# Optimization experiments

Hardware: AMD Instinct MI355X
Metric: run time of the kernel (lower is better)

Reference implementation:

```python
import jax, jax.numpy as jnp
import numpy as np

B = 256          # batch of images
TOK = 256        # 16x16 tokens per image
V = 1024         # codebook size
D = 256          # code dim


def setup_inputs() -> dict:
    key = jax.random.key(0)
    k1, k2, k3, k4 = jax.random.split(key, 4)
    image_seq = jax.random.randint(k1, (B, TOK), 0, V, dtype=jnp.int64)
    image_seq2 = jax.random.randint(k2, (B, TOK), 0, V, dtype=jnp.int64)
    alpha = jax.random.uniform(k3, (1,), dtype=jnp.float32)
    W = jax.random.normal(k4, (V, D), dtype=jnp.float32)
    return {"image_seq": image_seq, "image_seq2": image_seq2, "alpha": alpha, "W": W}


def reference(image_seq, image_seq2, alpha, W):
    a = alpha[0]
    # gather codebook entries: [B, TOK, D]
    emb = W[image_seq]
    emb2 = W[image_seq2]
    x = (1.0 - a) * emb + a * emb2
    xf = x.reshape(-1, D)                        # [N, D], N = B*TOK
    # brute-force L2 distance to every code, without materializing [N, V, D]:
    d = (jnp.sum(xf * xf, axis=-1, keepdims=True)
         - 2.0 * xf @ W.T
         + jnp.sum(W * W, axis=-1)[None, :])
    idx = jnp.argmin(d, axis=1)                  # top-1 nearest code, [N]
    # get_codebook_entry: gather, reshape to bhwc, permute to bchw
    z_q = W[idx].reshape(B, 16, 16, D)           # [B, 16, 16, 256]
    z_q = jnp.transpose(z_q, (0, 3, 1, 2))       # [B, 256, 16, 16]
    return z_q
```

## Files before the change

kernel.cpp:

```cpp
#include <hip/hip_runtime.h>

static constexpr int Vn = 1024;
static constexpr int Dn = 256;
static constexpr int NT = 65536;

typedef float vfloat4 __attribute__((ext_vector_type(4)));

__global__ __launch_bounds__(256) void gram_kernel(const float* __restrict__ W,
                                                   float* __restrict__ G,
                                                   float* __restrict__ norms) {
    __shared__ float As[32][33];
    __shared__ float Bs[32][33];
    const int tid = threadIdx.x;
    const int tx = tid & 15;
    const int ty = tid >> 4;
    const int bm = blockIdx.y * 32;
    const int bn = blockIdx.x * 32;
    float acc[2][2] = {};
    for (int k0 = 0; k0 < Dn; k0 += 32) {
#pragma unroll
        for (int s = 0; s < 4; ++s) {
            const int e = tid + 256 * s;
            const int m = e >> 5;
            const int k = e & 31;
            As[k][m] = W[(bm + m) * Dn + k0 + k];
            Bs[k][m] = W[(bn + m) * Dn + k0 + k];
        }
        __syncthreads();
#pragma unroll
        for (int kk = 0; kk < 32; ++kk) {
            float a[2], b[2];
#pragma unroll
            for (int u = 0; u < 2; ++u) a[u] = As[kk][ty + 16 * u];
#pragma unroll
            for (int w = 0; w < 2; ++w) b[w] = Bs[kk][tx + 16 * w];
#pragma unroll
            for (int u = 0; u < 2; ++u)
#pragma unroll
                for (int w = 0; w < 2; ++w)
                    acc[u][w] = fmaf(a[u], b[w], acc[u][w]);
        }
        __syncthreads();
    }
#pragma unroll
    for (int u = 0; u < 2; ++u) {
        const int row = bm + ty + 16 * u;
#pragma unroll
        for (int w = 0; w < 2; ++w) {
            const int col = bn + tx + 16 * w;
            G[row * Vn + col] = acc[u][w];
            if (row == col) norms[row] = acc[u][w];
        }
    }
}

__global__ __launch_bounds__(256) void argmin_write_kernel(const int* __restrict__ seq,
                                                           const int* __restrict__ seq2,
                                                           const float* __restrict__ alpha,
                                                           const float* __restrict__ G,
                                                           const float* __restrict__ norms,
                                                           const float* __restrict__ W,
                                                           float* __restrict__ out) {
    __shared__ float T[32][129];
    __shared__ int bestVs[32];
    const int tid = threadIdx.x;
    const int wave = tid >> 6;
    const int lane = tid & 63;
    const int t0 = blockIdx.x * 32;

    float4 nn_r[4];
#pragma unroll
    for (int s = 0; s < 4; ++s) nn_r[s] = ((const float4*)norms)[s * 64 + lane];

    const float a = alpha[0];
    const float c0 = -2.0f * (1.0f - a);
    const float c1 = -2.0f * a;

    for (int bb = 0; bb < 2; ++bb) {
        const int base_t = t0 + wave * 8 + bb * 4;
        const int base_l = wave * 8 + bb * 4;
        int iv[4], jv[4];
#pragma unroll
        for (int q = 0; q < 4; ++q) { iv[q] = seq[base_t + q]; jv[q] = seq2[base_t + q]; }
#pragma unroll
        for (int pair = 0; pair < 2; ++pair) {
            const int qa = pair * 2, qb = pair * 2 + 1;
            const float4* GiA = (const float4*)(G + iv[qa] * Vn);
            const float4* GjA = (const float4*)(G + jv[qa] * Vn);
            const float4* GiB = (const float4*)(G + iv[qb] * Vn);
            const float4* GjB = (const float4*)(G + jv[qb] * Vn);
            float4 gia[4], gja[4], gib[4], gjb[4];
#pragma unroll
            for (int s = 0; s < 4; ++s) {
                const int e = s * 64 + lane;
                gia[s] = GiA[e];
                gja[s] = GjA[e];
                gib[s] = GiB[e];
                gjb[s] = GjB[e];
            }
            float bestA = __builtin_inff(), bestB = __builtin_inff();
            int vA = 0, vB = 0;
#pragma unroll
            for (int s = 0; s < 4; ++s) {
                const int e = s * 64 + lane;
                const float4 nn = nn_r[s];
                const int v = e * 4;
                {
                    const float s0 = fmaf(c1, gja[s].x, fmaf(c0, gia[s].x, nn.x));
                    const float s1 = fmaf(c1, gja[s].y, fmaf(c0, gia[s].y, nn.y));
                    const float s2 = fmaf(c1, gja[s].z, fmaf(c0, gia[s].z, nn.z));
                    const float s3 = fmaf(c1, gja[s].w, fmaf(c0, gia[s].w, nn.w));
                    if (s0 < bestA) { bestA = s0; vA = v; }
                    if (s1 < bestA) { bestA = s1; vA = v + 1; }
                    if (s2 < bestA) { bestA = s2; vA = v + 2; }
                    if (s3 < bestA) { bestA = s3; vA = v + 3; }
                }
                {
                    const float s0 = fmaf(c1, gjb[s].x, fmaf(c0, gib[s].x, nn.x));
                    const float s1 = fmaf(c1, gjb[s].y, fmaf(c0, gib[s].y, nn.y));
                    const float s2 = fmaf(c1, gjb[s].z, fmaf(c0, gib[s].z, nn.z));
                    const float s3 = fmaf(c1, gjb[s].w, fmaf(c0, gib[s].w, nn.w));
                    if (s0 < bestB) { bestB = s0; vB = v; }
                    if (s1 < bestB) { bestB = s1; vB = v + 1; }
                    if (s2 < bestB) { bestB = s2; vB = v + 2; }
                    if (s3 < bestB) { bestB = s3; vB = v + 3; }
                }
            }
#pragma unroll
            for (int off = 32; off >= 1; off >>= 1) {
                const float oa = __shfl_down(bestA, off, 64);
                const int   va = __shfl_down(vA, off, 64);
                if (oa < bestA || (oa == bestA && va < vA)) { bestA = oa; vA = va; }
                const float ob = __shfl_down(bestB, off, 64);
                const int   vb = __shfl_down(vB, off, 64);
                if (ob < bestB || (ob == bestB && vb < vB)) { bestB = ob; vB = vb; }
            }
            if (lane == 0) {
                bestVs[base_l + qa] = vA;
                bestVs[base_l + qb] = vB;
            }
        }
    }
    __syncthreads();

    const int b   = t0 >> 8;
    const int hw0 = t0 & 255;
    float* outb = out + b * 65536 + hw0;
    const int tok = tid >> 3;
    const int l8  = tid & 7;
    const int hw4  = (tid & 7) * 4;
    const int drow = tid >> 3;
#pragma unroll
    for (int half = 0; half < 2; ++half) {
        const int v = bestVs[tok];
        const float4* Wr = (const float4*)(W + v * Dn + half * 128);
#pragma unroll
        for (int p = 0; p < 4; ++p) {
            const int d4 = p * 8 + l8;
            const float4 w4 = Wr[d4];
            T[tok][d4 * 4 + 0] = w4.x;
            T[tok][d4 * 4 + 1] = w4.y;
            T[tok][d4 * 4 + 2] = w4.z;
            T[tok][d4 * 4 + 3] = w4.w;
        }
        __syncthreads();
#pragma unroll
        for (int dp = 0; dp < 128; dp += 32) {
            const int dl = dp + drow;
            const int d = half * 128 + dl;
            vfloat4 o;
            o.x = T[hw4 + 0][dl];
            o.y = T[hw4 + 1][dl];
            o.z = T[hw4 + 2][dl];
            o.w = T[hw4 + 3][dl];
            __builtin_nontemporal_store(o, (vfloat4*)(outb + d * 256 + hw4));
        }
        __syncthreads();
    }
}

extern "C" void kernel_launch(void* const* d_in, const int* in_sizes, int n_in,
                              void* d_out, int out_size, void* d_ws, size_t ws_size,
                              hipStream_t stream) {
    const int*   seq   = (const int*)d_in[0];
    const int*   seq2  = (const int*)d_in[1];
    const float* alpha = (const float*)d_in[2];
    const float* W     = (const float*)d_in[3];
    float* out = (float*)d_out;

    char* ws = (char*)d_ws;
    float* G     = (float*)(ws);
    float* norms = (float*)(ws + 4194304);

    gram_kernel<<<dim3(32, 32), 256, 0, stream>>>(W, G, norms);
    argmin_write_kernel<<<NT / 32, 256, 0, stream>>>(seq, seq2, alpha, G, norms, W, out);
}
```

Before: 130.6 us.

## Enlarge Gram kernel tiles to 64x64 with register prefetch and vector loads

```diff
diff --git a/kernel.cpp b/kernel.cpp
--- a/kernel.cpp
+++ b/kernel.cpp
@@ -9,48 +9,70 @@
 __global__ __launch_bounds__(256) void gram_kernel(const float* __restrict__ W,
                                                    float* __restrict__ G,
                                                    float* __restrict__ norms) {
-    __shared__ float As[32][33];
-    __shared__ float Bs[32][33];
+    __shared__ float As[64][33];
+    __shared__ float Bs[64][33];
     const int tid = threadIdx.x;
     const int tx = tid & 15;
     const int ty = tid >> 4;
-    const int bm = blockIdx.y * 32;
-    const int bn = blockIdx.x * 32;
-    float acc[2][2] = {};
-    for (int k0 = 0; k0 < Dn; k0 += 32) {
-#pragma unroll
-        for (int s = 0; s < 4; ++s) {
-            const int e = tid + 256 * s;
-            const int m = e >> 5;
-            const int k = e & 31;
-            As[k][m] = W[(bm + m) * Dn + k0 + k];
-            Bs[k][m] = W[(bn + m) * Dn + k0 + k];
-        }
-        __syncthreads();
+    const int bm = blockIdx.y * 64;
+    const int bn = blockIdx.x * 64;
+    const float4* Wv = (const float4*)W;
+
+    const int m0  = tid >> 3;
+    const int kql = tid & 7;
+
+    float4 pa[2], pb[2];
+#pragma unroll
+    for (int s = 0; s < 2; ++s) {
+        pa[s] = Wv[(bm + m0 + 32 * s) * 64 + kql];
+        pb[s] = Wv[(bn + m0 + 32 * s) * 64 + kql];
+    }
+
+    float acc[4][4] = {};
+    for (int c = 0; c < 8; ++c) {
+#pragma unroll
+        for (int s = 0; s < 2; ++s) {
+            const int m = m0 + 32 * s;
+            As[m][kql * 4 + 0] = pa[s].x;
+            As[m][kql * 4 + 1] = pa[s].y;
+            As[m][kql * 4 + 2] = pa[s].z;
+            As[m][kql * 4 + 3] = pa[s].w;
+            Bs[m][kql * 4 + 0] = pb[s].x;
+            Bs[m][kql * 4 + 1] = pb[s].y;
+            Bs[m][kql * 4 + 2] = pb[s].z;
+            Bs[m][kql * 4 + 3] = pb[s].w;
+        }
+        __syncthreads();
+        if (c < 7) {
+            const int kq = (c + 1) * 8 + kql;
+#pragma unroll
+            for (int s = 0; s < 2; ++s) {
+                pa[s] = Wv[(bm + m0 + 32 * s) * 64 + kq];
+                pb[s] = Wv[(bn + m0 + 32 * s) * 64 + kq];
+            }
+        }
 #pragma unroll
         for (int kk = 0; kk < 32; ++kk) {
-            float a[2], b[2];
-#pragma unroll
-            for (int u = 0; u < 2; ++u) a[u] = As[kk][ty + 16 * u];
-#pragma unroll
-            for (int w = 0; w < 2; ++w) b[w] = Bs[kk][tx + 16 * w];
-#pragma unroll
-            for (int u = 0; u < 2; ++u)
-#pragma unroll
-                for (int w = 0; w < 2; ++w)
+            float a[4], b[4];
+#pragma unroll
+            for (int u = 0; u < 4; ++u) a[u] = As[ty * 4 + u][kk];
+#pragma unroll
+            for (int w = 0; w < 4; ++w) b[w] = Bs[tx * 4 + w][kk];
+#pragma unroll
+            for (int u = 0; u < 4; ++u)
+#pragma unroll
+                for (int w = 0; w < 4; ++w)
                     acc[u][w] = fmaf(a[u], b[w], acc[u][w]);
         }
         __syncthreads();
     }
 #pragma unroll
-    for (int u = 0; u < 2; ++u) {
-        const int row = bm + ty + 16 * u;
-#pragma unroll
-        for (int w = 0; w < 2; ++w) {
-            const int col = bn + tx + 16 * w;
-            G[row * Vn + col] = acc[u][w];
-            if (row == col) norms[row] = acc[u][w];
-        }
+    for (int u = 0; u < 4; ++u) {
+        const int row = bm + ty * 4 + u;
+        vfloat4 o;
+        o.x = acc[u][0]; o.y = acc[u][1]; o.z = acc[u][2]; o.w = acc[u][3];
+        *(vfloat4*)(G + row * Vn + bn + tx * 4) = o;
+        if (bm == bn && tx == ty) norms[row] = acc[u][u];
     }
 }
 
@@ -192,6 +214,6 @@
     float* G     = (float*)(ws);
     float* norms = (float*)(ws + 4194304);
 
-    gram_kernel<<<dim3(32, 32), 256, 0, stream>>>(W, G, norms);
+    gram_kernel<<<dim3(16, 16), 256, 0, stream>>>(W, G, norms);
     argmin_write_kernel<<<NT / 32, 256, 0, stream>>>(seq, seq2, alpha, G, norms, W, out);
 }
```

New measurement: 129.1 us. About the same (-1.1%).
